# Optimization experiments

Measured on AMD Instinct MI355X. Metric: run time of the kernel, lower is better.

Reference implementation:

```python
import jax, jax.numpy as jnp
import numpy as np

THRE = 0.5        # communication threshold
ALPHA = 0.8       # S_e / S_c mix in pattern gate
P_BIAS, P_WEIGHT = 0.1, 0.9
DILATE_K = 3
EPS = 1e-6


def warp_affine(src, M, out_hw):
    """torch F.affine_grid + F.grid_sample (bilinear, zeros padding, align_corners=False).
    src: (B,C,Hs,Ws), M: (B,2,3) normalized affine. Returns (B,C,Ho,Wo)."""
    B, C, Hs, Ws = src.shape
    Ho, Wo = out_hw
    xs = 2.0 * (jnp.arange(Wo, dtype=src.dtype) + 0.5) / Wo - 1.0
    ys = 2.0 * (jnp.arange(Ho, dtype=src.dtype) + 0.5) / Ho - 1.0
    gx, gy = jnp.meshgrid(xs, ys)                                   # (Ho,Wo)
    base = jnp.stack([gx, gy, jnp.ones_like(gx)], axis=-1)          # (Ho,Wo,3)
    g = jnp.einsum('bij,hwj->bhwi', M.astype(src.dtype), base)      # (B,Ho,Wo,2) x,y
    px = ((g[..., 0] + 1.0) * Ws - 1.0) * 0.5
    py = ((g[..., 1] + 1.0) * Hs - 1.0) * 0.5
    x0 = jnp.floor(px); y0 = jnp.floor(py)
    wx1 = px - x0; wx0 = 1.0 - wx1
    wy1 = py - y0; wy0 = 1.0 - wy1
    bidx = jnp.arange(B)[:, None, None]
    def samp(yi, xi):
        yi = yi.astype(jnp.int32); xi = xi.astype(jnp.int32)
        valid = (yi >= 0) & (yi < Hs) & (xi >= 0) & (xi < Ws)
        yc = jnp.clip(yi, 0, Hs - 1); xc = jnp.clip(xi, 0, Ws - 1)
        v = src[bidx, :, yc, xc]                                    # (B,Ho,Wo,C)
        return v * valid[..., None].astype(src.dtype)
    out = (samp(y0, x0) * (wy0 * wx0)[..., None]
         + samp(y0, x0 + 1) * (wy0 * wx1)[..., None]
         + samp(y0 + 1, x0) * (wy1 * wx0)[..., None]
         + samp(y0 + 1, x0 + 1) * (wy1 * wx1)[..., None])
    return jnp.transpose(out, (0, 3, 1, 2))


def masked_quantile(xf, mf, q):
    """torch.quantile(x[mask], q) with linear interpolation. xf:(N,HW) float, mf:(N,HW) bool."""
    xs = jnp.sort(jnp.where(mf, xf, jnp.inf), axis=-1)
    cnt = mf.sum(axis=-1)
    pos = q * jnp.maximum(cnt - 1, 0).astype(xf.dtype)
    lo = jnp.floor(pos).astype(jnp.int32)
    hi = jnp.ceil(pos).astype(jnp.int32)
    frac = pos - lo.astype(xf.dtype)
    vlo = jnp.take_along_axis(xs, lo[:, None], axis=-1)[:, 0]
    vhi = jnp.take_along_axis(xs, hi[:, None], axis=-1)[:, 0]
    val = vlo + frac * (vhi - vlo)
    return jnp.where(cnt > 0, val, jnp.zeros_like(val))


def qnorm01(x, mask, ql=0.2, qh=0.8):
    """_qnorm01_masked: per-image masked quantile normalization to [0,1]."""
    N = x.shape[0]
    xf = x.reshape(N, -1)
    mf = mask.reshape(N, -1) > 0
    lo = masked_quantile(xf, mf, ql)[:, None]
    hi = masked_quantile(xf, mf, qh)[:, None]
    y = jnp.clip((xf - lo) / (hi - lo + EPS), 0.0, 1.0) * mf.astype(x.dtype)
    return y.reshape(x.shape)


def pattern_gate(conf_b, feats_b, vis_b):
    """_build_pattern_gate. Returns P (1,1,H,W) on ego plane."""
    visf = (vis_b > 0).astype(feats_b.dtype)
    energy = jnp.mean(feats_b ** 2, axis=1, keepdims=True)          # (N,1,H,W)
    S_e = qnorm01(energy, vis_b) * visf
    S_c_raw = jnp.max(jax.nn.sigmoid(conf_b), axis=1, keepdims=True)  # A>1 branch
    S_c = qnorm01(S_c_raw, vis_b) * visf
    S_mix = ALPHA * S_e + (1.0 - ALPHA) * S_c
    D_e = qnorm01(1.0 - S_e[0:1], vis_b[0:1])
    D_c = qnorm01(1.0 - S_c[0:1], vis_b[0:1])
    D = (0.7 * D_e + 0.3 * D_c) * visf[0:1]
    m0 = vis_b[0:1].reshape(1, -1) > 0
    q20_e = masked_quantile(S_e[0:1].reshape(1, -1), m0, 0.2)[0]
    q20_c = masked_quantile(S_c[0:1].reshape(1, -1), m0, 0.2)[0]
    Ke = (S_e[0:1] <= q20_e) & (vis_b[0:1] > 0)
    Kc = (S_c[0:1] <= q20_c) & (vis_b[0:1] > 0)
    K_empty = (Ke & Kc).astype(feats_b.dtype)
    Sup_nei = jnp.mean(S_mix[1:] * visf[1:], axis=0, keepdims=True)
    P = D * Sup_nei * (1.0 - K_empty)
    return qnorm01(P, vis_b[0:1]) * visf[0:1]


def dilate(mask, k):
    if k <= 1:
        return mask
    return jax.lax.reduce_window(mask, -jnp.inf, jax.lax.max,
                                 (1, 1, k, k), (1, 1, 1, 1), 'SAME')


def owner_for_batch(feats_b, conf_b, vis_b, base_b):
    """_compute_owner_masks_from_comm for one batch group (N agents), eval mode
    (soft_tau=0 -> hard argmax owner), dual_ratio=0, dilate_k=3, supply='cls'."""
    N = feats_b.shape[0]
    visf = (vis_b > 0).astype(feats_b.dtype)
    S_full = jnp.clip(conf_b, 0.0, 1.0).mean(axis=1, keepdims=True) * visf
    P = pattern_gate(conf_b, feats_b, vis_b)                        # (1,1,H,W)
    S_b = S_full * (P_BIAS + P_WEIGHT * P)                          # broadcast over N
    scores = S_b * visf                                             # (N,1,H,W)
    winner = jnp.argmax(scores, axis=0)                             # (1,H,W)
    onehot = (jnp.arange(N)[:, None, None, None] == winner[None]).astype(feats_b.dtype)
    owner = onehot * (base_b > 0).astype(feats_b.dtype)
    return dilate(owner, DILATE_K)


def forward(x, psm_single, record_len, normalized_affine_matrix):
    B, L = normalized_affine_matrix.shape[:2]
    N = L  # uniform record_len assumed (record_len[b] == L for all b)
    sumN, C, H, W = x.shape
    A = psm_single.shape[1]
    # ego-view warp matrices t_matrix[0, :N] per batch, flattened to (B*N,2,3)
    M = normalized_affine_matrix[:, 0].reshape(B * N, 2, 3)
    ones = jnp.ones((B * N, 1, H, W), x.dtype)
    vis = warp_affine(ones, M, (H, W))          # warp masks
    conf = warp_affine(psm_single, M, (H, W))   # warped confidence maps
    wx = warp_affine(x, M, (H, W))              # warped features
    # Communication: where2comm-style threshold on max-sigmoid confidence; ego always ones
    comm_map = jnp.max(jax.nn.sigmoid(conf), axis=1, keepdims=True)
    comm = (comm_map > THRE).astype(x.dtype)
    comm = comm.reshape(B, N, 1, H, W).at[:, 0].set(1.0)            # (B,N,1,H,W)
    owner = jax.vmap(owner_for_batch)(
        wx.reshape(B, N, C, H, W), conf.reshape(B, N, A, H, W),
        vis.reshape(B, N, 1, H, W), comm)                           # (B,N,1,H,W)
    final = comm * owner
    wxm = wx.reshape(B, N, C, H, W) * final
    # effective rate over non-ego agents
    eff = final[:, 1:].sum(axis=(1, 2, 3, 4)) / ((N - 1) * H * W)
    effective_rate = eff.mean()
    x_out = wxm.max(axis=1)                                         # MaxFusion over agents
    return x_out, effective_rate


def setup_inputs():
    key = jax.random.key(0)
    k1, k2, k3 = jax.random.split(key, 3)
    B, N, C, A, H, W = 4, 5, 64, 2, 128, 256
    x = jax.random.normal(k1, (B * N, C, H, W), jnp.float32)
    psm_single = jax.random.normal(k2, (B * N, A, H, W), jnp.float32)
    record_len = jnp.full((B,), N, jnp.int32)
    eye = jnp.tile(jnp.array([[1.0, 0.0, 0.0], [0.0, 1.0, 0.0]], jnp.float32), (B, N, N, 1, 1))
    mats = eye + 0.05 * jax.random.normal(k3, (B, N, N, 2, 3), jnp.float32)
    return {"x": x, "psm_single": psm_single, "record_len": record_len,
            "normalized_affine_matrix": mats}


def reference(x, psm_single, record_len, normalized_affine_matrix):
    return forward(x, psm_single, record_len, normalized_affine_matrix)
```

## Files before the change

kernel.cpp:

```cpp
#include <hip/hip_runtime.h>

#define W_    256
#define H_    128
#define HW_   32768
#define NB    4
#define NA    5
#define NC    64
#define NIMG  20
#define EPS_  1e-6f

#define TW    32
#define TH    32
#define CAP   3072
#define TRIPS 12

struct Taps { int o00,o01,o10,o11; float w00,w01,w10,w11; };
struct TapsC { int cy0,cy1,cx0,cx1; float w00,w01,w10,w11; };

__device__ inline TapsC make_taps_c(float M0,float M1,float M2,float M3,float M4,float M5,
                                    int h, int w){
  float gx = 2.0f*((float)w+0.5f)/(float)W_ - 1.0f;
  float gy = 2.0f*((float)h+0.5f)/(float)H_ - 1.0f;
  float X = M0*gx + M1*gy + M2;
  float Y = M3*gx + M4*gy + M5;
  float px = ((X+1.0f)*(float)W_ - 1.0f)*0.5f;
  float py = ((Y+1.0f)*(float)H_ - 1.0f)*0.5f;
  float x0f = floorf(px), y0f = floorf(py);
  float wx1 = px-x0f, wy1 = py-y0f;
  float wx0 = 1.0f-wx1, wy0 = 1.0f-wy1;
  int x0=(int)x0f, y0=(int)y0f, x1=x0+1, y1=y0+1;
  bool vx0=(x0>=0)&&(x0<W_), vx1=(x1>=0)&&(x1<W_);
  bool vy0=(y0>=0)&&(y0<H_), vy1=(y1>=0)&&(y1<H_);
  TapsC t;
  t.cx0=min(max(x0,0),W_-1); t.cx1=min(max(x1,0),W_-1);
  t.cy0=min(max(y0,0),H_-1); t.cy1=min(max(y1,0),H_-1);
  t.w00=(vy0&&vx0)?(wy0*wx0):0.f;
  t.w01=(vy0&&vx1)?(wy0*wx1):0.f;
  t.w10=(vy1&&vx0)?(wy1*wx0):0.f;
  t.w11=(vy1&&vx1)?(wy1*wx1):0.f;
  return t;
}

__device__ inline Taps make_taps(const float* __restrict__ M, int h, int w){
  TapsC c = make_taps_c(M[0],M[1],M[2],M[3],M[4],M[5],h,w);
  Taps t;
  t.o00=c.cy0*W_+c.cx0; t.o01=c.cy0*W_+c.cx1; t.o10=c.cy1*W_+c.cx0; t.o11=c.cy1*W_+c.cx1;
  t.w00=c.w00; t.w01=c.w01; t.w10=c.w10; t.w11=c.w11;
  return t;
}

__device__ inline void proj_pt(float M0,float M1,float M2,float M3,float M4,float M5,
                               int h,int w,float&px,float&py){
  float gx = 2.0f*((float)w+0.5f)/(float)W_ - 1.0f;
  float gy = 2.0f*((float)h+0.5f)/(float)H_ - 1.0f;
  float X = M0*gx + M1*gy + M2;
  float Y = M3*gx + M4*gy + M5;
  px = ((X+1.0f)*(float)W_ - 1.0f)*0.5f;
  py = ((Y+1.0f)*(float)H_ - 1.0f)*0.5f;
}

__device__ inline float clip01(float v){ return fminf(fmaxf(v,0.f),1.f); }
__device__ inline float sigmoidf_(float v){
  if (v>=0.f){ float e=expf(-v); return 1.f/(1.f+e); }
  float e=expf(v); return e/(1.f+e);
}
__device__ inline float quantv(int cnt, float q, float vlo, float vhi){
  if (cnt<=0) return 0.f;
  float pos = q*(float)(cnt-1);
  float frac = pos - floorf(pos);
  return vlo + frac*(vhi-vlo);
}
__device__ inline float ge_f(float t, float lo, float hi){
  return clip01((t-lo)/(hi-lo+EPS_));
}

__device__ inline void gload4(const float* g, float* l){
  __builtin_amdgcn_global_load_lds(
      (const __attribute__((address_space(1))) void*)g,
      (__attribute__((address_space(3))) void*)l, 4, 0, 0);
}
#define SBAR __builtin_amdgcn_sched_barrier(0)

__global__ void k_init(int* counters){ if (threadIdx.x < 1+NIMG) counters[threadIdx.x] = 0; }

__global__ __launch_bounds__(256) void k_warp_stats(
  const float* __restrict__ x, const float* __restrict__ psm, const float* __restrict__ nam,
  float* __restrict__ vis, float* __restrict__ scraw, float* __restrict__ sfull,
  float* __restrict__ energy, int* __restrict__ cntv)
{
  __shared__ float smem[2][CAP];
  int tid = threadIdx.x;
  int tx = blockIdx.x, ty = blockIdx.y, bn = blockIdx.z;
  int b = bn/NA, n = bn - b*NA;
  const float* M = nam + (size_t)(b*NA*NA + n)*6;
  float M0=M[0],M1=M[1],M2=M[2],M3=M[3],M4=M[4],M5=M[5];
  int tw0 = tx*TW, th0 = ty*TH;
  int r  = tid>>3;
  int cb = (tid&7)<<2;
  int h  = th0 + r;
  int w0 = tw0 + cb;

  float pxa,pya,pxb,pyb,pxc,pyc,pxd,pyd;
  proj_pt(M0,M1,M2,M3,M4,M5, th0,      tw0,      pxa,pya);
  proj_pt(M0,M1,M2,M3,M4,M5, th0,      tw0+TW-1, pxb,pyb);
  proj_pt(M0,M1,M2,M3,M4,M5, th0+TH-1, tw0,      pxc,pyc);
  proj_pt(M0,M1,M2,M3,M4,M5, th0+TH-1, tw0+TW-1, pxd,pyd);
  float pxmin=fminf(fminf(pxa,pxb),fminf(pxc,pxd));
  float pxmax=fmaxf(fmaxf(pxa,pxb),fmaxf(pxc,pxd));
  float pymin=fminf(fminf(pya,pyb),fminf(pyc,pyd));
  float pymax=fmaxf(fmaxf(pya,pyb),fmaxf(pyc,pyd));
  int xs = min(max((int)floorf(pxmin)-1, 0), W_-1);
  int xe = min(max((int)floorf(pxmax)+2, 0), W_-1);
  int ys = min(max((int)floorf(pymin)-1, 0), H_-1);
  int ye = min(max((int)floorf(pymax)+2, 0), H_-1);
  int bw = xe-xs+1, bh = ye-ys+1;
  int E  = bh*bw;

  TapsC tc[4];
  #pragma unroll
  for (int k=0;k<4;++k) tc[k] = make_taps_c(M0,M1,M2,M3,M4,M5, h, w0+k);

  size_t idx = (size_t)bn*HW_ + (size_t)h*W_ + w0;
  float acc[4] = {0.f,0.f,0.f,0.f};

  if (E <= CAP){
    unsigned magic = (unsigned)((0x100000000ULL + (unsigned)bw - 1) / (unsigned)bw);
    const float* xb0 = x + (size_t)bn*NC*HW_ + (size_t)ys*W_ + xs;
    auto issue = [&](int ch, int bsel){
      const float* src = xb0 + (size_t)ch*HW_;
      float* dst = &smem[bsel][0];
      #pragma unroll
      for (int k=0;k<TRIPS;++k){
        int j  = tid + (k<<8);
        int jj = min(j, E-1);
        int row = (int)__umulhi((unsigned)jj, magic);
        int col = jj - row*bw;
        gload4(src + (size_t)row*W_ + col, dst + j);
      }
    };
    issue(0,0); issue(1,1);

    {
      const float* p0 = psm + ((size_t)bn*2+0)*HW_;
      const float* p1 = psm + ((size_t)bn*2+1)*HW_;
      int vsum = 0;
      #pragma unroll
      for (int k=0;k<4;++k){
        TapsC t = tc[k];
        int o00=t.cy0*W_+t.cx0, o01=t.cy0*W_+t.cx1, o10=t.cy1*W_+t.cx0, o11=t.cy1*W_+t.cx1;
        float vv = t.w00+t.w01+t.w10+t.w11;
        float c0 = t.w00*p0[o00]+t.w01*p0[o01]+t.w10*p0[o10]+t.w11*p0[o11];
        float c1 = t.w00*p1[o00]+t.w01*p1[o01]+t.w10*p1[o10]+t.w11*p1[o11];
        vis[idx+k]   = vv;
        scraw[idx+k] = fmaxf(sigmoidf_(c0), sigmoidf_(c1));
        sfull[idx+k] = (clip01(c0)+clip01(c1))*0.5f;
        vsum += (vv>0.f)?1:0;
      }
      #pragma unroll
      for (int off=32;off;off>>=1) vsum += __shfl_down(vsum,off);
      if ((tid&63)==0) atomicAdd(&cntv[bn], vsum);
    }

    int li00[4],li01[4],li10[4],li11[4];
    #pragma unroll
    for (int k=0;k<4;++k){
      li00[k]=(tc[k].cy0-ys)*bw + (tc[k].cx0-xs);
      li01[k]=(tc[k].cy0-ys)*bw + (tc[k].cx1-xs);
      li10[k]=(tc[k].cy1-ys)*bw + (tc[k].cx0-xs);
      li11[k]=(tc[k].cy1-ys)*bw + (tc[k].cx1-xs);
    }

    for (int c=0;c<NC;++c){
      asm volatile("s_waitcnt vmcnt(12)" ::: "memory"); SBAR;
      __builtin_amdgcn_s_barrier(); SBAR;
      const float* B = &smem[c&1][0];
      #pragma unroll
      for (int k=0;k<4;++k){
        float v = tc[k].w00*B[li00[k]] + tc[k].w01*B[li01[k]]
                + tc[k].w10*B[li10[k]] + tc[k].w11*B[li11[k]];
        acc[k] += v*v;
      }
      asm volatile("s_waitcnt lgkmcnt(0)" ::: "memory"); SBAR;
      __builtin_amdgcn_s_barrier(); SBAR;
      issue(min(c+2,NC-1), c&1);
    }
    asm volatile("s_waitcnt vmcnt(0)" ::: "memory");
  } else {
    const float* p0 = psm + ((size_t)bn*2+0)*HW_;
    const float* p1 = psm + ((size_t)bn*2+1)*HW_;
    int vsum = 0;
    int go00[4],go01[4],go10[4],go11[4];
    #pragma unroll
    for (int k=0;k<4;++k){
      TapsC t = tc[k];
      go00[k]=t.cy0*W_+t.cx0; go01[k]=t.cy0*W_+t.cx1;
      go10[k]=t.cy1*W_+t.cx0; go11[k]=t.cy1*W_+t.cx1;
      float vv = t.w00+t.w01+t.w10+t.w11;
      float c0 = t.w00*p0[go00[k]]+t.w01*p0[go01[k]]+t.w10*p0[go10[k]]+t.w11*p0[go11[k]];
      float c1 = t.w00*p1[go00[k]]+t.w01*p1[go01[k]]+t.w10*p1[go10[k]]+t.w11*p1[go11[k]];
      vis[idx+k]   = vv;
      scraw[idx+k] = fmaxf(sigmoidf_(c0), sigmoidf_(c1));
      sfull[idx+k] = (clip01(c0)+clip01(c1))*0.5f;
      vsum += (vv>0.f)?1:0;
    }
    #pragma unroll
    for (int off=32;off;off>>=1) vsum += __shfl_down(vsum,off);
    if ((tid&63)==0) atomicAdd(&cntv[bn], vsum);
    const float* xb = x + (size_t)bn*NC*HW_;
    for (int c=0;c<NC;++c){
      const float* pc = xb + (size_t)c*HW_;
      #pragma unroll
      for (int k=0;k<4;++k){
        float v = tc[k].w00*pc[go00[k]] + tc[k].w01*pc[go01[k]]
                + tc[k].w10*pc[go10[k]] + tc[k].w11*pc[go11[k]];
        acc[k] += v*v;
      }
    }
  }
  #pragma unroll
  for (int k=0;k<4;++k) energy[idx+k] = acc[k]*(1.0f/64.0f);
}

#define OS_T 1024
__global__ __launch_bounds__(1024) void k_select(
    const float* __restrict__ energy, const float* __restrict__ scraw,
    const float* __restrict__ ppre, const float* __restrict__ vis,
    const int* __restrict__ cnts,
    float* __restrict__ statsE, float* __restrict__ statsC, float* __restrict__ statsP,
    int mode)
{
  __shared__ int hist[16*256];
  __shared__ int cum[256];
  __shared__ unsigned s_pre;
  __shared__ int s_rk;
  int tid = threadIdx.x;
  int t = blockIdx.x;

  const float* d; const float* m; float* stats; int img, r, cnt;
  if (mode==0){
    bool isC = (t>=96); int tt = isC ? t-96 : t;
    if (tt<80){ img=tt>>2; r=tt&3; } else { int j=tt-80; img=(j>>2)*NA; r=4+(j&3); }
    d = (isC?scraw:energy) + (size_t)img*HW_;
    m = vis + (size_t)img*HW_;
    stats = isC?statsC:statsE;
    cnt = cnts[img];
  } else {
    img = t>>2; r = t&3;
    d = ppre + (size_t)img*HW_;
    m = vis + (size_t)(img*NA)*HW_;
    stats = statsP;
    cnt = cnts[img*NA];
  }
  int cm1 = cnt>0 ? cnt-1 : 0;
  float p2 = 0.2f*(float)cm1, p8 = 0.8f*(float)cm1;
  int l2=(int)floorf(p2), h2=(int)ceilf(p2), l8=(int)floorf(p8), h8=(int)ceilf(p8);
  int rank;
  switch(r){
    case 0: rank=l2; break;      case 1: rank=h2; break;
    case 2: rank=l8; break;      case 3: rank=h8; break;
    case 4: rank=cm1-l2; break;  case 5: rank=cm1-h2; break;
    case 6: rank=cm1-l8; break;  default: rank=cm1-h8; break;
  }

  unsigned key[32];
  #pragma unroll
  for (int k=0;k<32;++k){
    int i = tid + (k<<10);
    unsigned u = __float_as_uint(d[i]);
    unsigned kk = (u & 0x80000000u) ? ~u : (u|0x80000000u);
    key[k] = (m[i] > 0.f) ? kk : 0xFFFFFFFFu;
  }

  if (tid==0){ s_pre=0u; s_rk=rank; }
  int slice = tid & 15;
  #pragma unroll
  for (int round=0; round<4; ++round){
    const int shift = 24 - 8*round;
    for (int i=tid;i<16*256;i+=OS_T) hist[i]=0;
    __syncthreads();
    unsigned pre = s_pre;
    if (round==0){
      #pragma unroll
      for (int k=0;k<32;++k)
        atomicAdd(&hist[slice*256 + (key[k]>>24)], 1);
    } else {
      #pragma unroll
      for (int k=0;k<32;++k)
        if ((key[k]>>(shift+8)) == pre)
          atomicAdd(&hist[slice*256 + ((key[k]>>shift)&255u)], 1);
    }
    __syncthreads();
    if (tid<256){
      int tt=0;
      #pragma unroll
      for (int s=0;s<16;++s) tt += hist[s*256+tid];
      cum[tid]=tt;
    }
    __syncthreads();
    if (tid<64){
      int c0=cum[4*tid+0],c1=cum[4*tid+1],c2=cum[4*tid+2],c3=cum[4*tid+3];
      int i0=c0, i1=i0+c1, i2=i1+c2, i3=i2+c3;
      int tot=i3, scan=tot;
      #pragma unroll
      for (int off=1;off<64;off<<=1){ int v=__shfl_up(scan,off); if (tid>=off) scan+=v; }
      int base = scan-tot;
      int rk = s_rk; unsigned pr = s_pre;
      int b0=base, b1=base+i0, b2=base+i1, b3=base+i2, e3=base+i3;
      if      (rk>=b0 && rk<b1){ s_pre=(pr<<8)|(unsigned)(4*tid+0); s_rk=rk-b0; }
      else if (rk>=b1 && rk<b2){ s_pre=(pr<<8)|(unsigned)(4*tid+1); s_rk=rk-b1; }
      else if (rk>=b2 && rk<b3){ s_pre=(pr<<8)|(unsigned)(4*tid+2); s_rk=rk-b2; }
      else if (rk>=b3 && rk<e3){ s_pre=(pr<<8)|(unsigned)(4*tid+3); s_rk=rk-b3; }
    }
    __syncthreads();
  }
  if (tid==0){
    unsigned k = s_pre;
    unsigned u = (k & 0x80000000u) ? (k & 0x7FFFFFFFu) : ~k;
    stats[img*16 + 1 + r] = __uint_as_float(u);
    if (r==0) stats[img*16] = (float)cnt;
  }
}

__global__ void k_params(const float* __restrict__ statsE, const float* __restrict__ statsC,
                         float* __restrict__ params){
  int b = threadIdx.x;
  if (b>=NB) return;
  float* pr = params + b*32;
  for (int n=0;n<NA;++n){
    const float* sE = statsE + (size_t)(b*NA+n)*16;
    const float* sC = statsC + (size_t)(b*NA+n)*16;
    int cE=(int)sE[0], cC=(int)sC[0];
    pr[n]    = quantv(cE,0.2f,sE[1],sE[2]);
    pr[5+n]  = quantv(cE,0.8f,sE[3],sE[4]);
    pr[10+n] = quantv(cC,0.2f,sC[1],sC[2]);
    pr[15+n] = quantv(cC,0.8f,sC[3],sC[4]);
  }
  const float* sE0 = statsE + (size_t)(b*NA)*16;
  const float* sC0 = statsC + (size_t)(b*NA)*16;
  float loe=pr[0], hie=pr[5], loc=pr[10], hic=pr[15];
  float de_lo=0.f,de_hi=0.f,ke=0.f, dc_lo=0.f,dc_hi=0.f,kc=0.f;
  int c0=(int)sE0[0];
  if (c0>0){
    int cm1=c0-1;
    float pos2=0.2f*(float)cm1, pos8=0.8f*(float)cm1;
    float f2=pos2-floorf(pos2), f8=pos8-floorf(pos8);
    float a,bb;
    a=1.f-ge_f(sE0[5],loe,hie); bb=1.f-ge_f(sE0[6],loe,hie); de_lo=a+f2*(bb-a);
    a=1.f-ge_f(sE0[7],loe,hie); bb=1.f-ge_f(sE0[8],loe,hie); de_hi=a+f8*(bb-a);
    a=ge_f(sE0[1],loe,hie);     bb=ge_f(sE0[2],loe,hie);     ke  =a+f2*(bb-a);
  }
  int c0c=(int)sC0[0];
  if (c0c>0){
    int cm1=c0c-1;
    float pos2=0.2f*(float)cm1, pos8=0.8f*(float)cm1;
    float f2=pos2-floorf(pos2), f8=pos8-floorf(pos8);
    float a,bb;
    a=1.f-ge_f(sC0[5],loc,hic); bb=1.f-ge_f(sC0[6],loc,hic); dc_lo=a+f2*(bb-a);
    a=1.f-ge_f(sC0[7],loc,hic); bb=1.f-ge_f(sC0[8],loc,hic); dc_hi=a+f8*(bb-a);
    a=ge_f(sC0[1],loc,hic);     bb=ge_f(sC0[2],loc,hic);     kc  =a+f2*(bb-a);
  }
  pr[20]=de_lo; pr[21]=de_hi; pr[22]=dc_lo; pr[23]=dc_hi; pr[24]=ke; pr[25]=kc;
}

__global__ __launch_bounds__(256) void k_ppre(
  const float* __restrict__ vis, const float* __restrict__ scraw,
  const float* __restrict__ energy, const float* __restrict__ params,
  float* __restrict__ ppre)
{
  int w=threadIdx.x, h=blockIdx.x, b=blockIdx.y;
  int p=h*W_+w;
  const float* pr = params + b*32;
  size_t base = (size_t)b*NA*HW_ + p;
  float se[NA], sc[NA], vf[NA];
  #pragma unroll
  for (int n=0;n<NA;++n){
    float vv = vis[base + (size_t)n*HW_];
    float f = (vv>0.f)?1.f:0.f; vf[n]=f;
    se[n] = clip01((energy[base+(size_t)n*HW_]-pr[n])/(pr[5+n]-pr[n]+EPS_))*f;
    sc[n] = clip01((scraw[base+(size_t)n*HW_]-pr[10+n])/(pr[15+n]-pr[10+n]+EPS_))*f;
  }
  float sup = 0.f;
  #pragma unroll
  for (int n=1;n<NA;++n) sup += (0.8f*se[n]+0.2f*sc[n])*vf[n];
  sup *= 0.25f;
  float de = clip01(((1.f-se[0])-pr[20])/(pr[21]-pr[20]+EPS_))*vf[0];
  float dc = clip01(((1.f-sc[0])-pr[22])/(pr[23]-pr[22]+EPS_))*vf[0];
  float D  = (0.7f*de + 0.3f*dc)*vf[0];
  bool ke = (se[0] <= pr[24]) && (vf[0]>0.f);
  bool kc = (sc[0] <= pr[25]) && (vf[0]>0.f);
  float kem = (ke&&kc)?1.f:0.f;
  ppre[(size_t)b*HW_+p] = D*sup*(1.f-kem);
}

__global__ __launch_bounds__(256) void k_owner(
  const float* __restrict__ vis, const float* __restrict__ scraw,
  const float* __restrict__ sfull, const float* __restrict__ ppre,
  const float* __restrict__ statsP, int* __restrict__ omask)
{
  int w=threadIdx.x,h=blockIdx.x,b=blockIdx.y;
  int p=h*W_+w;
  const float* sP = statsP + b*16;
  int cntP=(int)sP[0];
  float plo = quantv(cntP,0.2f,sP[1],sP[2]);
  float phi = quantv(cntP,0.8f,sP[3],sP[4]);
  size_t base=(size_t)b*NA*HW_+p;
  float vf0 = (vis[base]>0.f)?1.f:0.f;
  float Pf = clip01((ppre[(size_t)b*HW_+p]-plo)/(phi-plo+EPS_))*vf0;
  float gate = 0.1f + 0.9f*Pf;
  int winner=0; float best=-1.f;
  int cbits=0;
  #pragma unroll
  for (int n=0;n<NA;++n){
    float vv = vis[base+(size_t)n*HW_];
    float f=(vv>0.f)?1.f:0.f;
    float s = ((sfull[base+(size_t)n*HW_]*f)*gate)*f;
    if (s>best){best=s;winner=n;}
    bool cm = (n==0) || (scraw[base+(size_t)n*HW_] > 0.5f);
    if (cm) cbits |= 1<<n;
  }
  int ob = ((cbits>>winner)&1) ? (1<<winner) : 0;
  omask[(size_t)b*HW_+p] = ob | (cbits<<8);
}

__global__ __launch_bounds__(256) void k_final(
  const int* __restrict__ omask, int* __restrict__ fmask, int* __restrict__ counter)
{
  int w=threadIdx.x,h=blockIdx.x,b=blockIdx.y;
  int p=h*W_+w;
  const int* om = omask + (size_t)b*HW_;
  int ow=0;
  #pragma unroll
  for (int dy=-1;dy<=1;++dy){
    int y=h+dy; if (y<0||y>=H_) continue;
    #pragma unroll
    for (int dx=-1;dx<=1;++dx){
      int x=w+dx; if (x<0||x>=W_) continue;
      ow |= om[y*W_+x];
    }
  }
  int cbits=(om[p]>>8)&31;
  int fin = ow & cbits & 31;
  fmask[(size_t)b*HW_+p]=fin;
  int cn = __popc(fin & 30);
  for (int off=32;off;off>>=1) cn += __shfl_down(cn,off);
  if ((threadIdx.x&63)==0) atomicAdd(counter, cn);
}

__global__ __launch_bounds__(256, 2) void k_out(
  const float* __restrict__ x, const float* __restrict__ nam,
  const int* __restrict__ fmask, const int* __restrict__ counter,
  float* __restrict__ out, int out_size)
{
  int w=threadIdx.x, h=blockIdx.x, b=blockIdx.y;
  int p=h*W_+w;
  int fin = fmask[(size_t)b*HW_+p] & 31;
  float init = (__popc(fin)<NA) ? 0.f : -__builtin_inff();
  Taps tp[NA];
  #pragma unroll
  for (int n=0;n<NA;++n) tp[n] = make_taps(nam + (size_t)(b*NA*NA+n)*6, h, w);
  #pragma unroll 1
  for (int cb=0; cb<NC/16; ++cb){
    float m[16];
    #pragma unroll
    for (int c=0;c<16;++c) m[c]=init;
    #pragma unroll
    for (int n=0;n<NA;++n){
      if (!((fin>>n)&1)) continue;
      const float* pc = x + ((size_t)(b*NA+n)*NC + cb*16)*HW_;
      float a00[16],a01[16],a10[16],a11[16];
      #pragma unroll
      for (int c=0;c<16;++c){
        a00[c]=pc[tp[n].o00]; a01[c]=pc[tp[n].o01]; a10[c]=pc[tp[n].o10]; a11[c]=pc[tp[n].o11];
        pc += HW_;
      }
      #pragma unroll
      for (int c=0;c<16;++c){
        float v = tp[n].w00*a00[c] + tp[n].w01*a01[c] + tp[n].w10*a10[c] + tp[n].w11*a11[c];
        m[c] = fmaxf(m[c], v);
      }
    }
    #pragma unroll
    for (int c=0;c<16;++c)
      out[(((size_t)b*NC + cb*16 + c)*H_+h)*W_+w] = m[c];
  }
  if (b==0 && h==0 && w==0)
    out[out_size-1] = (float)(*counter) * (1.0f/524288.0f);
}

extern "C" void kernel_launch(void* const* d_in, const int* in_sizes, int n_in,
                              void* d_out, int out_size, void* d_ws, size_t ws_size,
                              hipStream_t stream) {
  (void)in_sizes; (void)n_in; (void)ws_size;
  const float* x   = (const float*)d_in[0];
  const float* psm = (const float*)d_in[1];
  const float* nam = (const float*)d_in[3];
  float* out = (float*)d_out;

  float* ws     = (float*)d_ws;
  float* vis    = ws;
  float* scraw  = vis    + (size_t)NIMG*HW_;
  float* sfull  = scraw  + (size_t)NIMG*HW_;
  float* energy = sfull  + (size_t)NIMG*HW_;
  float* ppre   = energy + (size_t)NIMG*HW_;
  float* statsE = ppre   + (size_t)NB*HW_;
  float* statsC = statsE + NIMG*16;
  float* statsP = statsC + NIMG*16;
  float* params = statsP + NB*16;
  int*   omask  = (int*)(params + NB*32);
  int*   fmask  = omask + (size_t)NB*HW_;
  int*   counter= fmask + (size_t)NB*HW_;
  int*   cntv   = counter + 1;

  hipLaunchKernelGGL(k_init, dim3(1), dim3(64), 0, stream, counter);
  hipLaunchKernelGGL(k_warp_stats, dim3(W_/TW, H_/TH, NIMG), dim3(256), 0, stream,
                     x, psm, nam, vis, scraw, sfull, energy, cntv);
  hipLaunchKernelGGL(k_select, dim3(192), dim3(OS_T), 0, stream,
                     energy, scraw, ppre, vis, cntv, statsE, statsC, statsP, 0);
  hipLaunchKernelGGL(k_params, dim3(1), dim3(64), 0, stream, statsE, statsC, params);
  hipLaunchKernelGGL(k_ppre, dim3(H_,NB), dim3(W_), 0, stream,
                     vis, scraw, energy, params, ppre);
  hipLaunchKernelGGL(k_select, dim3(16), dim3(OS_T), 0, stream,
                     energy, scraw, ppre, vis, cntv, statsE, statsC, statsP, 1);
  hipLaunchKernelGGL(k_owner, dim3(H_,NB), dim3(W_), 0, stream,
                     vis, scraw, sfull, ppre, statsP, omask);
  hipLaunchKernelGGL(k_final, dim3(H_,NB), dim3(W_), 0, stream, omask, fmask, counter);
  hipLaunchKernelGGL(k_out, dim3(H_,NB), dim3(W_), 0, stream,
                     x, nam, fmask, counter, out, out_size);
}
```

Measured before the change: 247.1 us.

## Stage warp source tiles via float4 register loads with padded LDS pitch

Replaces the per-element global_load_lds staging of each channel's source bounding box with 16-byte vector loads into registers, then stores into a padded, 4-aligned shared-memory tile. The row pitch is padded to avoid LDS bank conflicts, and the next channel is prefetched into registers while the current one is sampled. The cost is two __syncthreads per channel and a wider aligned footprint that may push some tiles past CAP into the slow fallback path.

```diff
diff --git a/kernel.cpp b/kernel.cpp
--- a/kernel.cpp
+++ b/kernel.cpp
@@ -12,7 +12,7 @@
 #define TW    32
 #define TH    32
 #define CAP   3072
-#define TRIPS 12
+#define NCH   3
 
 struct Taps { int o00,o01,o10,o11; float w00,w01,w10,w11; };
 struct TapsC { int cy0,cy1,cx0,cx1; float w00,w01,w10,w11; };
@@ -74,13 +74,6 @@
   return clip01((t-lo)/(hi-lo+EPS_));
 }
 
-__device__ inline void gload4(const float* g, float* l){
-  __builtin_amdgcn_global_load_lds(
-      (const __attribute__((address_space(1))) void*)g,
-      (__attribute__((address_space(3))) void*)l, 4, 0, 0);
-}
-#define SBAR __builtin_amdgcn_sched_barrier(0)
-
 __global__ void k_init(int* counters){ if (threadIdx.x < 1+NIMG) counters[threadIdx.x] = 0; }
 
 __global__ __launch_bounds__(256) void k_warp_stats(
@@ -113,8 +106,13 @@
   int xe = min(max((int)floorf(pxmax)+2, 0), W_-1);
   int ys = min(max((int)floorf(pymin)-1, 0), H_-1);
   int ye = min(max((int)floorf(pymax)+2, 0), H_-1);
-  int bw = xe-xs+1, bh = ye-ys+1;
-  int E  = bh*bw;
+  int xs4 = xs & ~3;
+  int bwid = xe - xs4 + 1, bh = ye - ys + 1;
+  int nck = (bwid+3)>>2;
+  int bwp = nck<<2;
+  int pitch = bwp + 4;
+  if ((pitch & 31) == 0) pitch += 4;
+  int E2 = bh*pitch;
 
   TapsC tc[4];
   #pragma unroll
@@ -123,22 +121,24 @@
   size_t idx = (size_t)bn*HW_ + (size_t)h*W_ + w0;
   float acc[4] = {0.f,0.f,0.f,0.f};
 
-  if (E <= CAP){
-    unsigned magic = (unsigned)((0x100000000ULL + (unsigned)bw - 1) / (unsigned)bw);
-    const float* xb0 = x + (size_t)bn*NC*HW_ + (size_t)ys*W_ + xs;
-    auto issue = [&](int ch, int bsel){
-      const float* src = xb0 + (size_t)ch*HW_;
-      float* dst = &smem[bsel][0];
-      #pragma unroll
-      for (int k=0;k<TRIPS;++k){
-        int j  = tid + (k<<8);
-        int jj = min(j, E-1);
-        int row = (int)__umulhi((unsigned)jj, magic);
-        int col = jj - row*bw;
-        gload4(src + (size_t)row*W_ + col, dst + j);
-      }
-    };
-    issue(0,0); issue(1,1);
+  if (E2 <= CAP){
+    int totq = bh*nck;
+    unsigned magic = (unsigned)((0x100000000ULL + (unsigned)nck - 1) / (unsigned)nck);
+    const float* xb0 = x + (size_t)bn*NC*HW_ + (size_t)ys*W_ + xs4;
+
+    int qrow[NCH], qcol[NCH];
+    #pragma unroll
+    for (int k=0;k<NCH;++k){
+      int q = tid + (k<<8);
+      int qq = min(q, totq-1);
+      int row = (int)__umulhi((unsigned)qq, magic);
+      qrow[k] = row; qcol[k] = (qq - row*nck)<<2;
+    }
+
+    float4 rr[NCH];
+    #pragma unroll
+    for (int k=0;k<NCH;++k)
+      rr[k] = *reinterpret_cast<const float4*>(xb0 + (size_t)qrow[k]*W_ + qcol[k]);
 
     {
       const float* p0 = psm + ((size_t)bn*2+0)*HW_;
@@ -161,30 +161,44 @@
       if ((tid&63)==0) atomicAdd(&cntv[bn], vsum);
     }
 
+    #pragma unroll
+    for (int k=0;k<NCH;++k)
+      *reinterpret_cast<float4*>(&smem[0][qrow[k]*pitch + qcol[k]]) = rr[k];
+    __syncthreads();
+
     int li00[4],li01[4],li10[4],li11[4];
     #pragma unroll
     for (int k=0;k<4;++k){
-      li00[k]=(tc[k].cy0-ys)*bw + (tc[k].cx0-xs);
-      li01[k]=(tc[k].cy0-ys)*bw + (tc[k].cx1-xs);
-      li10[k]=(tc[k].cy1-ys)*bw + (tc[k].cx0-xs);
-      li11[k]=(tc[k].cy1-ys)*bw + (tc[k].cx1-xs);
-    }
-
+      li00[k]=(tc[k].cy0-ys)*pitch + (tc[k].cx0-xs4);
+      li01[k]=(tc[k].cy0-ys)*pitch + (tc[k].cx1-xs4);
+      li10[k]=(tc[k].cy1-ys)*pitch + (tc[k].cx0-xs4);
+      li11[k]=(tc[k].cy1-ys)*pitch + (tc[k].cx1-xs4);
+    }
+
+    #pragma unroll 1
     for (int c=0;c<NC;++c){
-      asm volatile("s_waitcnt vmcnt(12)" ::: "memory"); SBAR;
-      __builtin_amdgcn_s_barrier(); SBAR;
-      const float* B = &smem[c&1][0];
+      if (c+1 < NC){
+        const float* src = xb0 + (size_t)(c+1)*HW_;
+        #pragma unroll
+        for (int k=0;k<NCH;++k)
+          rr[k] = *reinterpret_cast<const float4*>(src + (size_t)qrow[k]*W_ + qcol[k]);
+      }
+      const float* B = smem[c&1];
       #pragma unroll
       for (int k=0;k<4;++k){
         float v = tc[k].w00*B[li00[k]] + tc[k].w01*B[li01[k]]
                 + tc[k].w10*B[li10[k]] + tc[k].w11*B[li11[k]];
         acc[k] += v*v;
       }
-      asm volatile("s_waitcnt lgkmcnt(0)" ::: "memory"); SBAR;
-      __builtin_amdgcn_s_barrier(); SBAR;
-      issue(min(c+2,NC-1), c&1);
-    }
-    asm volatile("s_waitcnt vmcnt(0)" ::: "memory");
+      if (c+1 < NC){
+        __syncthreads();
+        float* Bn = smem[(c+1)&1];
+        #pragma unroll
+        for (int k=0;k<NCH;++k)
+          *reinterpret_cast<float4*>(&Bn[qrow[k]*pitch + qcol[k]]) = rr[k];
+        __syncthreads();
+      }
+    }
   } else {
     const float* p0 = psm + ((size_t)bn*2+0)*HW_;
     const float* p1 = psm + ((size_t)bn*2+1)*HW_;
```

After: 339.9 us. 37.6% more time.
